# Kernel optimization log

Hardware: AMD Instinct MI355X
Metric: run time of the kernel (lower is better)

The kernel has to match this reference:

```python
import jax, jax.numpy as jnp
import numpy as np

B, H, S, D = 4, 16, 2048, 64
SCALE_FACTOR = 8.0  # forward arg; module multiplies qk by 1/scale_factor = 0.125 = 1/sqrt(D)
# dropout_p is an undefined global in the source module; treated as 0 (identity)
# for a deterministic reference.

def setup_inputs() -> dict:
    key0 = jax.random.key(0)
    kq, kk, kv = jax.random.split(key0, 3)
    query = jax.random.normal(kq, (B, H, S, D), dtype=jnp.float32)
    key = jax.random.normal(kk, (B, H, S, D), dtype=jnp.float32)
    value = jax.random.normal(kv, (B, H, S, D), dtype=jnp.float32)
    return {"query": query, "key": key, "value": value}

def reference(query, key, value):
    inv_scale = 1.0 / SCALE_FACTOR
    # [B,H,S,S] attention scores (the module materializes this full matrix)
    qk = jnp.einsum('bhqd,bhkd->bhqk', query, key) * inv_scale
    probs = jax.nn.softmax(qk, axis=-1)
    # dropout is identity (p effectively 0 / eval-mode deterministic baseline)
    out = jnp.einsum('bhqk,bhkd->bhqd', probs, value)
    return out
```

## Files before the change

kernel.cpp:

```cpp
#include <hip/hip_runtime.h>
#include <hip/hip_bf16.h>

#define SEQ 2048
#define DIMH 64
#define KB 64
#define NT (SEQ / KB)

typedef __attribute__((ext_vector_type(8))) short bf16x8;
typedef __attribute__((ext_vector_type(4))) float f32x4;

extern "C" __device__ float __ocml_native_exp2_f32(float);
#define EXP2(x) __ocml_native_exp2_f32(x)

__device__ inline unsigned short f2bf(float f) {
    union { __bf16 h; unsigned short u; } c;
    c.h = (__bf16)f;
    return c.u;
}
__device__ inline unsigned pack2(float a, float b) {
    return (unsigned)f2bf(a) | ((unsigned)f2bf(b) << 16);
}

__device__ inline int swz(int row, int col) {
    int g = (((row & 7) ^ ((row >> 3) & 7)) << 3);
    return row * 64 + (col ^ g);
}

__device__ inline void perm32swap(unsigned &a, unsigned &b) {
    asm("v_permlane32_swap_b32 %0, %1" : "+v"(a), "+v"(b));
}
__device__ inline void perm16swap(unsigned &a, unsigned &b) {
    asm("v_permlane16_swap_b32 %0, %1" : "+v"(a), "+v"(b));
}

__global__ __launch_bounds__(128, 2) void fattn(
    const float* __restrict__ Q, const float* __restrict__ K,
    const float* __restrict__ V, float* __restrict__ O)
{
    __shared__ __align__(16) unsigned short Ksh[2][KB * DIMH];
    __shared__ __align__(16) unsigned short Vt[2][KB * DIMH];

    const int tid  = threadIdx.x;
    const int lane = tid & 63;
    const int wv   = tid >> 6;

    const int bid = blockIdx.x;
    const int swb = (bid & 7) * 128 + (bid >> 3);
    const int bh  = swb >> 4;
    const int qt  = swb & 15;

    const int l15 = lane & 15;
    const int lg  = lane >> 4;

    const float* qh = Q + (size_t)bh * SEQ * DIMH;
    const float* kh = K + (size_t)bh * SEQ * DIMH;
    const float* vh = V + (size_t)bh * SEQ * DIMH;
    float*       oh = O + (size_t)bh * SEQ * DIMH;

    const int q0 = qt * 128 + wv * 64;

    int koff[4][2];
    #pragma unroll
    for (int n = 0; n < 4; ++n)
        #pragma unroll
        for (int ks = 0; ks < 2; ++ks)
            koff[n][ks] = swz(n * 16 + l15, ks * 32 + lg * 8);

    const int c4 = (tid & 15) * 4;
    const int rK = tid >> 4;
    int kstoff[8], vstoff[2][4];
    #pragma unroll
    for (int rr = 0; rr < 8; ++rr) kstoff[rr] = swz(rr * 8 + rK, c4);
    #pragma unroll
    for (int a = 0; a < 2; ++a)
        #pragma unroll
        for (int j = 0; j < 4; ++j)
            vstoff[a][j] = swz(c4 + j, a * 32 + rK * 4);

    const float QS = 0.180336880111120f;
    bf16x8 qf[4][2];
    #pragma unroll
    for (int h = 0; h < 4; ++h)
        #pragma unroll
        for (int ks = 0; ks < 2; ++ks) {
            const float* src = qh + (size_t)(q0 + h * 16 + l15) * DIMH + ks * 32 + lg * 8;
            f32x4 a = *reinterpret_cast<const f32x4*>(src);
            f32x4 b = *reinterpret_cast<const f32x4*>(src + 4);
            bf16x8 vq;
            #pragma unroll
            for (int j = 0; j < 4; ++j) {
                vq[j]     = (short)f2bf(a[j] * QS);
                vq[j + 4] = (short)f2bf(b[j] * QS);
            }
            qf[h][ks] = vq;
        }

    bf16x8 ones;
    #pragma unroll
    for (int j = 0; j < 8; ++j) ones[j] = (short)0x3F80;

    f32x4 oacc[4][4];
    #pragma unroll
    for (int h = 0; h < 4; ++h)
        #pragma unroll
        for (int d = 0; d < 4; ++d) oacc[h][d] = (f32x4){0.f, 0.f, 0.f, 0.f};
    f32x4 lacc[4] = {{0.f,0.f,0.f,0.f}, {0.f,0.f,0.f,0.f},
                     {0.f,0.f,0.f,0.f}, {0.f,0.f,0.f,0.f}};

    auto stage_tile = [&](int t, int b) {
        const size_t tb = (size_t)t * KB;
        #pragma unroll
        for (int rr = 0; rr < 8; ++rr) {
            const f32x4 k4 = *reinterpret_cast<const f32x4*>(
                kh + (tb + rr * 8 + rK) * DIMH + c4);
            uint2 kk;
            kk.x = pack2(k4[0], k4[1]);
            kk.y = pack2(k4[2], k4[3]);
            *reinterpret_cast<uint2*>(&Ksh[b][kstoff[rr]]) = kk;
        }
        #pragma unroll
        for (int a = 0; a < 2; ++a) {
            f32x4 v4[4];
            #pragma unroll
            for (int i = 0; i < 4; ++i)
                v4[i] = *reinterpret_cast<const f32x4*>(
                    vh + (tb + a * 32 + rK * 4 + i) * DIMH + c4);
            #pragma unroll
            for (int j = 0; j < 4; ++j) {
                uint2 w;
                w.x = pack2(v4[0][j], v4[1][j]);
                w.y = pack2(v4[2][j], v4[3][j]);
                *reinterpret_cast<uint2*>(&Vt[b][vstoff[a][j]]) = w;
            }
        }
    };

    stage_tile(0, 0);
    __syncthreads();

    for (int kt = 0; kt < NT; ++kt) {
        const int cur = kt & 1;
        const unsigned short* Kb = Ksh[cur];
        const unsigned short* Vb = Vt[cur];
        const bool pf = (kt + 1 < NT);

        if (pf) stage_tile(kt + 1, cur ^ 1);

        __builtin_amdgcn_s_setprio(1);

        bf16x8 pa[4][2];
        #pragma unroll
        for (int np = 0; np < 2; ++np) {
            unsigned u[4][4];
            #pragma unroll
            for (int nn = 0; nn < 2; ++nn) {
                const int n = np * 2 + nn;
                bf16x8 kf0 = *reinterpret_cast<const bf16x8*>(&Kb[koff[n][0]]);
                bf16x8 kf1 = *reinterpret_cast<const bf16x8*>(&Kb[koff[n][1]]);
                #pragma unroll
                for (int h = 0; h < 4; ++h) {
                    f32x4 a = {0.f, 0.f, 0.f, 0.f};
                    a = __builtin_amdgcn_mfma_f32_16x16x32_bf16(kf0, qf[h][0], a, 0, 0, 0);
                    a = __builtin_amdgcn_mfma_f32_16x16x32_bf16(kf1, qf[h][1], a, 0, 0, 0);
                    u[h][2 * nn]     = pack2(EXP2(a[0]), EXP2(a[1]));
                    u[h][2 * nn + 1] = pack2(EXP2(a[2]), EXP2(a[3]));
                }
            }
            #pragma unroll
            for (int h = 0; h < 4; ++h) {
                unsigned a0 = u[h][0], b0 = u[h][2];
                unsigned a1 = u[h][1], b1 = u[h][3];
                perm32swap(a0, b0); perm16swap(a0, b0);
                perm32swap(a1, b1); perm16swap(a1, b1);
                union { unsigned w[4]; bf16x8 v; } pu;
                pu.w[0] = a0; pu.w[1] = a1; pu.w[2] = b0; pu.w[3] = b1;
                pa[h][np] = pu.v;
            }
        }

        #pragma unroll
        for (int h = 0; h < 4; ++h) {
            lacc[h] = __builtin_amdgcn_mfma_f32_16x16x32_bf16(pa[h][0], ones, lacc[h], 0, 0, 0);
            lacc[h] = __builtin_amdgcn_mfma_f32_16x16x32_bf16(pa[h][1], ones, lacc[h], 0, 0, 0);
        }

        #pragma unroll
        for (int d = 0; d < 4; ++d) {
            bf16x8 vb0 = *reinterpret_cast<const bf16x8*>(&Vb[koff[d][0]]);
            bf16x8 vb1 = *reinterpret_cast<const bf16x8*>(&Vb[koff[d][1]]);
            #pragma unroll
            for (int h = 0; h < 4; ++h) {
                oacc[h][d] = __builtin_amdgcn_mfma_f32_16x16x32_bf16(pa[h][0], vb0, oacc[h][d], 0, 0, 0);
                oacc[h][d] = __builtin_amdgcn_mfma_f32_16x16x32_bf16(pa[h][1], vb1, oacc[h][d], 0, 0, 0);
            }
        }

        __builtin_amdgcn_s_setprio(0);

        if (pf) {
            asm volatile("s_waitcnt lgkmcnt(0)" ::: "memory");
            __builtin_amdgcn_s_barrier();
            asm volatile("" ::: "memory");
        }
    }

    #pragma unroll
    for (int h = 0; h < 4; ++h)
        #pragma unroll
        for (int r = 0; r < 4; ++r) {
            float inv = 1.0f / lacc[h][r];
            float* dst = oh + (size_t)(q0 + h * 16 + lg * 4 + r) * DIMH;
            #pragma unroll
            for (int d = 0; d < 4; ++d)
                dst[d * 16 + l15] = oacc[h][d][r] * inv;
        }
}

extern "C" void kernel_launch(void* const* d_in, const int* in_sizes, int n_in,
                              void* d_out, int out_size, void* d_ws, size_t ws_size,
                              hipStream_t stream) {
    const float* q = (const float*)d_in[0];
    const float* k = (const float*)d_in[1];
    const float* v = (const float*)d_in[2];
    float* out = (float*)d_out;
    dim3 grid(64 * (SEQ / 128));
    dim3 block(128);
    fattn<<<grid, block, 0, stream>>>(q, k, v, out);
}
```

Measured before the change: 102.2 us.

## Use 256-thread blocks with 128-key tiles processed as two sub-tiles

Doubles the query rows per block (4 waves, 256 queries) and the key tile to 128 rows, so each staged K/V tile is shared by twice as many waves and there are half as many barriers per head. The transposed V layout is widened to 128 columns with its own swizzle, and the inner loop walks two 64-key sub-tiles. This cuts global reloads and bf16 conversion of K/V per query, at the cost of doubled LDS use and a grid of only 512 blocks, which may reduce occupancy and load balance.

```diff
diff --git a/kernel.cpp b/kernel.cpp
--- a/kernel.cpp
+++ b/kernel.cpp
@@ -3,7 +3,7 @@
 
 #define SEQ 2048
 #define DIMH 64
-#define KB 64
+#define KB 128
 #define NT (SEQ / KB)
 
 typedef __attribute__((ext_vector_type(8))) short bf16x8;
@@ -21,10 +21,14 @@
     return (unsigned)f2bf(a) | ((unsigned)f2bf(b) << 16);
 }
 
-__device__ inline int swz(int row, int col) {
+__device__ inline int swzK(int row, int col) {
     int g = (((row & 7) ^ ((row >> 3) & 7)) << 3);
     return row * 64 + (col ^ g);
 }
+__device__ inline int swzV(int row, int col) {
+    int g = (((row & 7) ^ ((row >> 3) & 7)) << 3);
+    return row * 128 + (col ^ g);
+}
 
 __device__ inline void perm32swap(unsigned &a, unsigned &b) {
     asm("v_permlane32_swap_b32 %0, %1" : "+v"(a), "+v"(b));
@@ -33,21 +37,21 @@
     asm("v_permlane16_swap_b32 %0, %1" : "+v"(a), "+v"(b));
 }
 
-__global__ __launch_bounds__(128, 2) void fattn(
+__global__ __launch_bounds__(256, 2) void fattn(
     const float* __restrict__ Q, const float* __restrict__ K,
     const float* __restrict__ V, float* __restrict__ O)
 {
     __shared__ __align__(16) unsigned short Ksh[2][KB * DIMH];
-    __shared__ __align__(16) unsigned short Vt[2][KB * DIMH];
+    __shared__ __align__(16) unsigned short Vt[2][DIMH * KB];
 
     const int tid  = threadIdx.x;
     const int lane = tid & 63;
     const int wv   = tid >> 6;
 
     const int bid = blockIdx.x;
-    const int swb = (bid & 7) * 128 + (bid >> 3);
-    const int bh  = swb >> 4;
-    const int qt  = swb & 15;
+    const int swb = (bid & 7) * 64 + (bid >> 3);
+    const int bh  = swb >> 3;
+    const int qt  = swb & 7;
 
     const int l15 = lane & 15;
     const int lg  = lane >> 4;
@@ -57,25 +61,27 @@
     const float* vh = V + (size_t)bh * SEQ * DIMH;
     float*       oh = O + (size_t)bh * SEQ * DIMH;
 
-    const int q0 = qt * 128 + wv * 64;
-
-    int koff[4][2];
+    const int q0 = qt * 256 + wv * 64;
+
+    int koff[4][2], vtoff[4][2];
     #pragma unroll
     for (int n = 0; n < 4; ++n)
         #pragma unroll
-        for (int ks = 0; ks < 2; ++ks)
-            koff[n][ks] = swz(n * 16 + l15, ks * 32 + lg * 8);
+        for (int ks = 0; ks < 2; ++ks) {
+            koff[n][ks]  = swzK(n * 16 + l15, ks * 32 + lg * 8);
+            vtoff[n][ks] = swzV(n * 16 + l15, ks * 32 + lg * 8);
+        }
 
     const int c4 = (tid & 15) * 4;
     const int rK = tid >> 4;
     int kstoff[8], vstoff[2][4];
     #pragma unroll
-    for (int rr = 0; rr < 8; ++rr) kstoff[rr] = swz(rr * 8 + rK, c4);
+    for (int rr = 0; rr < 8; ++rr) kstoff[rr] = swzK(rr * 16 + rK, c4);
     #pragma unroll
     for (int a = 0; a < 2; ++a)
         #pragma unroll
         for (int j = 0; j < 4; ++j)
-            vstoff[a][j] = swz(c4 + j, a * 32 + rK * 4);
+            vstoff[a][j] = swzV(c4 + j, a * 64 + rK * 4);
 
     const float QS = 0.180336880111120f;
     bf16x8 qf[4][2];
@@ -112,7 +118,7 @@
         #pragma unroll
         for (int rr = 0; rr < 8; ++rr) {
             const f32x4 k4 = *reinterpret_cast<const f32x4*>(
-                kh + (tb + rr * 8 + rK) * DIMH + c4);
+                kh + (tb + rr * 16 + rK) * DIMH + c4);
             uint2 kk;
             kk.x = pack2(k4[0], k4[1]);
             kk.y = pack2(k4[2], k4[3]);
@@ -124,7 +130,7 @@
             #pragma unroll
             for (int i = 0; i < 4; ++i)
                 v4[i] = *reinterpret_cast<const f32x4*>(
-                    vh + (tb + a * 32 + rK * 4 + i) * DIMH + c4);
+                    vh + (tb + a * 64 + rK * 4 + i) * DIMH + c4);
             #pragma unroll
             for (int j = 0; j < 4; ++j) {
                 uint2 w;
@@ -140,58 +146,63 @@
 
     for (int kt = 0; kt < NT; ++kt) {
         const int cur = kt & 1;
-        const unsigned short* Kb = Ksh[cur];
-        const unsigned short* Vb = Vt[cur];
+        const unsigned short* Kbase = Ksh[cur];
+        const unsigned short* Vbase = Vt[cur];
         const bool pf = (kt + 1 < NT);
 
         if (pf) stage_tile(kt + 1, cur ^ 1);
 
         __builtin_amdgcn_s_setprio(1);
 
-        bf16x8 pa[4][2];
-        #pragma unroll
-        for (int np = 0; np < 2; ++np) {
-            unsigned u[4][4];
-            #pragma unroll
-            for (int nn = 0; nn < 2; ++nn) {
-                const int n = np * 2 + nn;
-                bf16x8 kf0 = *reinterpret_cast<const bf16x8*>(&Kb[koff[n][0]]);
-                bf16x8 kf1 = *reinterpret_cast<const bf16x8*>(&Kb[koff[n][1]]);
+        #pragma unroll
+        for (int sub = 0; sub < 2; ++sub) {
+            const unsigned short* Kb = &Kbase[sub * 4096];
+
+            bf16x8 pa[4][2];
+            #pragma unroll
+            for (int np = 0; np < 2; ++np) {
+                unsigned u[4][4];
+                #pragma unroll
+                for (int nn = 0; nn < 2; ++nn) {
+                    const int n = np * 2 + nn;
+                    bf16x8 kf0 = *reinterpret_cast<const bf16x8*>(&Kb[koff[n][0]]);
+                    bf16x8 kf1 = *reinterpret_cast<const bf16x8*>(&Kb[koff[n][1]]);
+                    #pragma unroll
+                    for (int h = 0; h < 4; ++h) {
+                        f32x4 a = {0.f, 0.f, 0.f, 0.f};
+                        a = __builtin_amdgcn_mfma_f32_16x16x32_bf16(kf0, qf[h][0], a, 0, 0, 0);
+                        a = __builtin_amdgcn_mfma_f32_16x16x32_bf16(kf1, qf[h][1], a, 0, 0, 0);
+                        u[h][2 * nn]     = pack2(EXP2(a[0]), EXP2(a[1]));
+                        u[h][2 * nn + 1] = pack2(EXP2(a[2]), EXP2(a[3]));
+                    }
+                }
                 #pragma unroll
                 for (int h = 0; h < 4; ++h) {
-                    f32x4 a = {0.f, 0.f, 0.f, 0.f};
-                    a = __builtin_amdgcn_mfma_f32_16x16x32_bf16(kf0, qf[h][0], a, 0, 0, 0);
-                    a = __builtin_amdgcn_mfma_f32_16x16x32_bf16(kf1, qf[h][1], a, 0, 0, 0);
-                    u[h][2 * nn]     = pack2(EXP2(a[0]), EXP2(a[1]));
-                    u[h][2 * nn + 1] = pack2(EXP2(a[2]), EXP2(a[3]));
+                    unsigned a0 = u[h][0], b0 = u[h][2];
+                    unsigned a1 = u[h][1], b1 = u[h][3];
+                    perm32swap(a0, b0); perm16swap(a0, b0);
+                    perm32swap(a1, b1); perm16swap(a1, b1);
+                    union { unsigned w[4]; bf16x8 v; } pu;
+                    pu.w[0] = a0; pu.w[1] = a1; pu.w[2] = b0; pu.w[3] = b1;
+                    pa[h][np] = pu.v;
                 }
             }
+
             #pragma unroll
             for (int h = 0; h < 4; ++h) {
-                unsigned a0 = u[h][0], b0 = u[h][2];
-                unsigned a1 = u[h][1], b1 = u[h][3];
-                perm32swap(a0, b0); perm16swap(a0, b0);
-                perm32swap(a1, b1); perm16swap(a1, b1);
-                union { unsigned w[4]; bf16x8 v; } pu;
-                pu.w[0] = a0; pu.w[1] = a1; pu.w[2] = b0; pu.w[3] = b1;
-                pa[h][np] = pu.v;
-            }
-        }
-
-        #pragma unroll
-        for (int h = 0; h < 4; ++h) {
-            lacc[h] = __builtin_amdgcn_mfma_f32_16x16x32_bf16(pa[h][0], ones, lacc[h], 0, 0, 0);
-            lacc[h] = __builtin_amdgcn_mfma_f32_16x16x32_bf16(pa[h][1], ones, lacc[h], 0, 0, 0);
-        }
-
-        #pragma unroll
-        for (int d = 0; d < 4; ++d) {
-            bf16x8 vb0 = *reinterpret_cast<const bf16x8*>(&Vb[koff[d][0]]);
-            bf16x8 vb1 = *reinterpret_cast<const bf16x8*>(&Vb[koff[d][1]]);
-            #pragma unroll
-            for (int h = 0; h < 4; ++h) {
-                oacc[h][d] = __builtin_amdgcn_mfma_f32_16x16x32_bf16(pa[h][0], vb0, oacc[h][d], 0, 0, 0);
-                oacc[h][d] = __builtin_amdgcn_mfma_f32_16x16x32_bf16(pa[h][1], vb1, oacc[h][d], 0, 0, 0);
+                lacc[h] = __builtin_amdgcn_mfma_f32_16x16x32_bf16(pa[h][0], ones, lacc[h], 0, 0, 0);
+                lacc[h] = __builtin_amdgcn_mfma_f32_16x16x32_bf16(pa[h][1], ones, lacc[h], 0, 0, 0);
+            }
+
+            #pragma unroll
+            for (int d = 0; d < 4; ++d) {
+                bf16x8 vb0 = *reinterpret_cast<const bf16x8*>(&Vbase[vtoff[d][0] + sub * 64]);
+                bf16x8 vb1 = *reinterpret_cast<const bf16x8*>(&Vbase[vtoff[d][1] + sub * 64]);
+                #pragma unroll
+                for (int h = 0; h < 4; ++h) {
+                    oacc[h][d] = __builtin_amdgcn_mfma_f32_16x16x32_bf16(pa[h][0], vb0, oacc[h][d], 0, 0, 0);
+                    oacc[h][d] = __builtin_amdgcn_mfma_f32_16x16x32_bf16(pa[h][1], vb1, oacc[h][d], 0, 0, 0);
+                }
             }
         }
 
@@ -223,7 +234,7 @@
     const float* k = (const float*)d_in[1];
     const float* v = (const float*)d_in[2];
     float* out = (float*)d_out;
-    dim3 grid(64 * (SEQ / 128));
-    dim3 block(128);
+    dim3 grid(64 * (SEQ / 256));
+    dim3 block(256);
     fattn<<<grid, block, 0, stream>>>(q, k, v, out);
 }
```

New measurement: 93.63 us. 8.4% less time.
